# Kernel optimization log

Measured on AMD Instinct MI355X. Metric: run time of the kernel, lower is better.

Reference implementation:

```python
import itertools
import jax, jax.numpy as jnp
import numpy as np

N, C, D, S = 512, 128, 16, 10  # atoms, channels, irreps dim (0e+1o+2e+3o), species
IR_DIMS = {'0e': 1, '1o': 3}
MULS = {'0e': (23, 4, 1), '1o': (33, 6, 1)}  # path multiplicities for orders (3, 2, 1)


def _make_u(key, order, mul, ir_dim):
    # Synthetic stand-in for e3nn.reduced_symmetric_tensor_product_basis:
    # under permutation of the `order` leading D axes.
    shape = (D,) * order + (mul, ir_dim)
    u = jax.random.normal(key, shape, dtype=jnp.float32)
    mask = jax.random.bernoulli(jax.random.fold_in(key, 1), 0.1, shape)
    u = jnp.where(mask, u, 0.0)
    perms = list(itertools.permutations(range(order)))
    u = sum(jnp.transpose(u, p + (order, order + 1)) for p in perms) / len(perms)
    return u


def setup_inputs() -> dict:
    key = jax.random.key(0)
    ks = jax.random.split(key, 16)
    inp = {
        'x': jax.random.normal(ks[0], (N, C, D), dtype=jnp.float32),
        'index': jax.random.randint(ks[1], (N,), 0, S, dtype=jnp.int32),
    }
    i = 2
    for ir in IR_DIMS:
        for order, mul in zip((3, 2, 1), MULS[ir]):
            inp[f'u{order}_{ir}'] = _make_u(ks[i], order, mul, IR_DIMS[ir]); i += 1
            # gradient_normalization='element' -> init stddev mul**-0.5, no runtime scale
            inp[f'w{order}_{ir}'] = (jax.random.normal(ks[i], (S, mul, C), dtype=jnp.float32)
                                     * mul ** -0.5); i += 1
    return inp


def _contract(x, idx, u3, u2, u1, w3, w2, w1):
    # x: (N,C,D); uK: (D,)*K + (mulK, ir); wK: (S, mulK, C)
    w3i, w2i, w1i = w3[idx], w2[idx], w1[idx]  # species gather -> (N, mulK, C)
    # order 3: einsum('...jki,kc,cj->c...i', u3, w3i, x) batched over atoms.
    # Form p[n,c,k,j] = w3i[n,k,c]*x[n,c,j] first (small), then one big contraction.
    p = jnp.einsum('nkc,ncj->nckj', w3i, x)              # (N,C,mul3,D)
    out = jnp.einsum('abjki,nckj->ncabi', u3, p)         # (N,C,D,D,ir)
    # order 2: accumulate U2.w2, then contract one D axis with x
    out = out + jnp.einsum('abki,nkc->ncabi', u2, w2i)   # (N,C,D,D,ir)
    out = jnp.einsum('ncaji,ncj->ncai', out, x)          # (N,C,D,ir)
    # order 1: accumulate U1.w1, then final contraction with x
    out = out + jnp.einsum('aki,nkc->ncai', u1, w1i)     # (N,C,D,ir)
    out = jnp.einsum('ncji,ncj->nci', out, x)            # (N,C,ir)
    return out


def reference(x, index, u3_0e, w3_0e, u2_0e, w2_0e, u1_0e, w1_0e,
              u3_1o, w3_1o, u2_1o, w2_1o, u1_1o, w1_1o):
    out0 = _contract(x, index, u3_0e, u2_0e, u1_0e, w3_0e, w2_0e, w1_0e)  # (N,C,1)
    out1 = _contract(x, index, u3_1o, u2_1o, u1_1o, w3_1o, w2_1o, w1_1o)  # (N,C,3)
    return jnp.concatenate([out0, out1], axis=-1)  # (N,C,4) irreps 0e+1o
```

## Files before the change

kernel.cpp:

```cpp
#include <hip/hip_runtime.h>


#define DD     16
#define NATOM  512
#define NCH    128
#define NSPEC  10
#define NT3    816
#define NT2    136
#define NT     968
#define NTP    1024
#define ATB    16
#define APT    4
#define MAXB   42
#define CHUNKS 8
#define NTC    128
#define TILE   16
#define NTILES (NTC / TILE)
#define TPW    (TILE / 4)
#define CHALF  2
#define CT     8

#define WS_DESC  0
#define WS_ORDER 1024
#define WS_COEF  8192
#define COEF_BYTES (NSPEC * NTP * NCH * 16)
#define WS_PART  (WS_COEF + COEF_BYTES)

struct TermTable { unsigned v[NTP]; };
constexpr TermTable build_terms() {
  TermTable T{};
  int t = 0;
  for (int a = 0; a < DD; a++)
    for (int b = a; b < DD; b++)
      for (int j = b; j < DD; j++) {
        unsigned m = (a == b && b == j) ? 1u : ((a == b || b == j) ? 3u : 6u);
        T.v[t++] = (unsigned)(a | (b << 5) | (j << 10) | (3u << 15) | (m << 18));
      }
  for (int a = 0; a < DD; a++)
    for (int b = a; b < DD; b++) {
      unsigned m = (a == b) ? 1u : 2u;
      T.v[t++] = (unsigned)(a | (b << 5) | (16 << 10) | (2u << 15) | (m << 18));
    }
  for (int a = 0; a < DD; a++)
    T.v[t++] = (unsigned)(a | (16 << 5) | (16 << 10) | (1u << 15) | (1u << 18));
  while (t < NTP) T.v[t++] = (unsigned)(17 | (17 << 5) | (17 << 10));
  return T;
}
constexpr TermTable TERMS = build_terms();

__device__ void do_setup(const int* __restrict__ index, int* __restrict__ desc,
                         int* __restrict__ order) {
  __shared__ int cnt[NSPEC], cursor[NSPEC], bbase[NSPEC + 1];
  const int tid = threadIdx.x;
  if (tid < NSPEC) { cnt[tid] = 0; cursor[tid] = 0; }
  __syncthreads();
  for (int i = tid; i < NATOM; i += 128) atomicAdd(&cnt[index[i]], 1);
  for (int i = tid; i < MAXB * ATB; i += 128) order[i] = -1;
  __syncthreads();
  if (tid == 0) {
    int base = 0;
    for (int s = 0; s < NSPEC; s++) { bbase[s] = base; base += (cnt[s] + ATB - 1) / ATB; }
    bbase[NSPEC] = base;
  }
  __syncthreads();
  for (int i = tid; i < NATOM; i += 128) {
    int s = index[i];
    int pos = atomicAdd(&cursor[s], 1);
    order[bbase[s] * ATB + pos] = i;
  }
  for (int i = tid; i < MAXB; i += 128) {
    int sp = -1;
    for (int s = 0; s < NSPEC; s++)
      if (i >= bbase[s] && i < bbase[s + 1]) sp = s;
    desc[i] = sp;
  }
}

__global__ __launch_bounds__(128) void coef_setup_kernel(
    const float* __restrict__ u3_0, const float* __restrict__ w3_0,
    const float* __restrict__ u2_0, const float* __restrict__ w2_0,
    const float* __restrict__ u1_0, const float* __restrict__ w1_0,
    const float* __restrict__ u3_1, const float* __restrict__ w3_1,
    const float* __restrict__ u2_1, const float* __restrict__ w2_1,
    const float* __restrict__ u1_1, const float* __restrict__ w1_1,
    const int* __restrict__ index, int* __restrict__ desc,
    int* __restrict__ order, float* __restrict__ coef) {
  if (blockIdx.y == NTP / CT) {
    if (blockIdx.x == 0) do_setup(index, desc, order);
    return;
  }
  const int s = blockIdx.x;
  const int c = threadIdx.x;
  const int tbase = blockIdx.y * CT;

  __shared__ float us0[CT][23];
  __shared__ float us1[CT][99];

  for (int i = 0; i < CT; ++i) {
    const unsigned ev = TERMS.v[tbase + i];
    const int kind = (ev >> 15) & 7;
    const int a = ev & 31, b = (ev >> 5) & 31, j = (ev >> 10) & 31;
    if (kind == 3) {
      const int off = (a * DD + b) * DD + j;
      if (c < 23) us0[i][c] = u3_0[off * 23 + c];
      else if (c < 122) us1[i][c - 23] = u3_1[(size_t)off * 99 + (c - 23)];
    } else if (kind == 2) {
      const int off = a * DD + b;
      if (c < 4) us0[i][c] = u2_0[off * 4 + c];
      else if (c < 22) us1[i][c - 4] = u2_1[off * 18 + (c - 4)];
    } else if (kind == 1) {
      if (c < 1) us0[i][0] = u1_0[a];
      else if (c < 4) us1[i][c - 1] = u1_1[a * 3 + (c - 1)];
    }
  }
  __syncthreads();

  float r3_0[23], r3_1[33], r2_0[4], r2_1[6];
#pragma unroll
  for (int k = 0; k < 23; k++) r3_0[k] = w3_0[(s * 23 + k) * NCH + c];
#pragma unroll
  for (int k = 0; k < 33; k++) r3_1[k] = w3_1[(s * 33 + k) * NCH + c];
#pragma unroll
  for (int k = 0; k < 4; k++) r2_0[k] = w2_0[(s * 4 + k) * NCH + c];
#pragma unroll
  for (int k = 0; k < 6; k++) r2_1[k] = w2_1[(s * 6 + k) * NCH + c];
  const float r1_0 = w1_0[s * NCH + c];
  const float r1_1 = w1_1[s * NCH + c];

  for (int i = 0; i < CT; ++i) {
    const unsigned ev = TERMS.v[tbase + i];
    const int kind = (ev >> 15) & 7;
    const float fm = (float)((ev >> 18) & 7);
    float s0 = 0.f, s1 = 0.f, s2 = 0.f, s3 = 0.f;
    if (kind == 3) {
#pragma unroll
      for (int k = 0; k < 23; k++) s0 += us0[i][k] * r3_0[k];
#pragma unroll
      for (int k = 0; k < 33; k++) {
        const float w = r3_1[k];
        s1 += us1[i][k * 3 + 0] * w;
        s2 += us1[i][k * 3 + 1] * w;
        s3 += us1[i][k * 3 + 2] * w;
      }
    } else if (kind == 2) {
#pragma unroll
      for (int k = 0; k < 4; k++) s0 += us0[i][k] * r2_0[k];
#pragma unroll
      for (int k = 0; k < 6; k++) {
        const float w = r2_1[k];
        s1 += us1[i][k * 3 + 0] * w;
        s2 += us1[i][k * 3 + 1] * w;
        s3 += us1[i][k * 3 + 2] * w;
      }
    } else if (kind == 1) {
      s0 = us0[i][0] * r1_0;
      s1 = us1[i][0] * r1_1;
      s2 = us1[i][1] * r1_1;
      s3 = us1[i][2] * r1_1;
    }
    *(float4*)(coef + ((size_t)(s * NTP + tbase + i) * NCH + c) * 4) =
        float4{fm * s0, fm * s1, fm * s2, fm * s3};
  }
}

__device__ __forceinline__ void stage_tile(const float* __restrict__ lane_base,
                                           int t0_tile, float* dst_base, int wave) {
#pragma unroll
  for (int r = 0; r < TPW; ++r) {
    const int term = wave * TPW + r;
    const float* g = lane_base + (size_t)(t0_tile + term) * (NCH * 4);
    float* l = dst_base + term * 256;
    __builtin_amdgcn_global_load_lds(
        (const __attribute__((address_space(1))) unsigned int*)g,
        (__attribute__((address_space(3))) unsigned int*)l, 16, 0, 0);
  }
}

template <int CH>
__device__ __forceinline__ void eval_chunk(const float* __restrict__ lane_base,
                                           float (*lbuf)[TILE * 256],
                                           int wave, int lane,
                                           const float (&xr)[APT][18],
                                           float (&ac)[APT][4]) {
  constexpr int T0 = CH * NTC;
  stage_tile(lane_base, T0, &lbuf[0][0], wave);
#pragma unroll
  for (int tile = 0; tile < NTILES; ++tile) {
    __syncthreads();
    if (tile + 1 < NTILES)
      stage_tile(lane_base, T0 + (tile + 1) * TILE, &lbuf[(tile + 1) & 1][0], wave);
    const float* lb = &lbuf[tile & 1][0];
#pragma unroll
    for (int i = 0; i < TILE; ++i) {
      const unsigned ev = TERMS.v[T0 + tile * TILE + i];
      const int ea = ev & 31, eb = (ev >> 5) & 31, ej = (ev >> 10) & 31;
      const float4 cf = *(const float4*)(lb + (i * 64 + lane) * 4);
#pragma unroll
      for (int k = 0; k < APT; ++k) {
        const float m = xr[k][ea] * xr[k][eb] * xr[k][ej];
        ac[k][0] += cf.x * m; ac[k][1] += cf.y * m;
        ac[k][2] += cf.z * m; ac[k][3] += cf.w * m;
      }
    }
  }
}

__device__ __forceinline__ void load16(float (&xr)[18], const float* __restrict__ p) {
  const float4* q = (const float4*)p;
  const float4 v0 = q[0], v1 = q[1], v2 = q[2], v3 = q[3];
  xr[0] = v0.x; xr[1] = v0.y; xr[2] = v0.z; xr[3] = v0.w;
  xr[4] = v1.x; xr[5] = v1.y; xr[6] = v1.z; xr[7] = v1.w;
  xr[8] = v2.x; xr[9] = v2.y; xr[10] = v2.z; xr[11] = v2.w;
  xr[12] = v3.x; xr[13] = v3.y; xr[14] = v3.z; xr[15] = v3.w;
}

__global__ __launch_bounds__(256, 4) void contract_kernel(const float* __restrict__ x,
                                                          const int* __restrict__ desc,
                                                          const int* __restrict__ order,
                                                          const float* __restrict__ coef,
                                                          float* __restrict__ partial) {
  const int s = desc[blockIdx.x];
  if (s < 0) return;
  const int lane = threadIdx.x & 63;
  const int wave = threadIdx.x >> 6;
  const int c = blockIdx.z * 64 + lane;

  __shared__ float lbuf[2][TILE * 256];

  int n[APT];
#pragma unroll
  for (int k = 0; k < APT; k++) n[k] = order[blockIdx.x * ATB + wave * APT + k];

  float xr[APT][18];
#pragma unroll
  for (int k = 0; k < APT; k++) {
#pragma unroll
    for (int i = 0; i < DD; i++) xr[k][i] = 0.f;
    xr[k][16] = 1.f;
    xr[k][17] = 0.f;
  }
#pragma unroll
  for (int k = 0; k < APT; k++)
    if (n[k] >= 0) load16(xr[k], x + ((size_t)n[k] * NCH + c) * DD);

  float ac[APT][4];
#pragma unroll
  for (int k = 0; k < APT; k++) { ac[k][0] = 0.f; ac[k][1] = 0.f; ac[k][2] = 0.f; ac[k][3] = 0.f; }

  const float* lane_base = coef + ((size_t)s * NTP * NCH + (size_t)blockIdx.z * 64 + lane) * 4;

  switch (blockIdx.y) {
    case 0: eval_chunk<0>(lane_base, lbuf, wave, lane, xr, ac); break;
    case 1: eval_chunk<1>(lane_base, lbuf, wave, lane, xr, ac); break;
    case 2: eval_chunk<2>(lane_base, lbuf, wave, lane, xr, ac); break;
    case 3: eval_chunk<3>(lane_base, lbuf, wave, lane, xr, ac); break;
    case 4: eval_chunk<4>(lane_base, lbuf, wave, lane, xr, ac); break;
    case 5: eval_chunk<5>(lane_base, lbuf, wave, lane, xr, ac); break;
    case 6: eval_chunk<6>(lane_base, lbuf, wave, lane, xr, ac); break;
    default: eval_chunk<7>(lane_base, lbuf, wave, lane, xr, ac); break;
  }

  float* pb = partial + (size_t)blockIdx.y * (NATOM * NCH * 4);
#pragma unroll
  for (int k = 0; k < APT; k++)
    if (n[k] >= 0)
      *(float4*)(pb + ((size_t)n[k] * NCH + c) * 4) =
          float4{ac[k][0], ac[k][1], ac[k][2], ac[k][3]};
}

__global__ __launch_bounds__(256) void reduce_kernel(const float4* __restrict__ partial,
                                                     float4* __restrict__ out) {
  const int i = blockIdx.x * 256 + threadIdx.x;
  float4 s{0.f, 0.f, 0.f, 0.f};
#pragma unroll
  for (int ch = 0; ch < CHUNKS; ch++) {
    const float4 v = partial[(size_t)ch * (NATOM * NCH) + i];
    s.x += v.x; s.y += v.y; s.z += v.z; s.w += v.w;
  }
  out[i] = s;
}

extern "C" void kernel_launch(void* const* d_in, const int* in_sizes, int n_in,
                              void* d_out, int out_size, void* d_ws, size_t ws_size,
                              hipStream_t stream) {
  const float* x    = (const float*)d_in[0];
  const int* index  = (const int*)d_in[1];
  const float* u3_0 = (const float*)d_in[2];
  const float* w3_0 = (const float*)d_in[3];
  const float* u2_0 = (const float*)d_in[4];
  const float* w2_0 = (const float*)d_in[5];
  const float* u1_0 = (const float*)d_in[6];
  const float* w1_0 = (const float*)d_in[7];
  const float* u3_1 = (const float*)d_in[8];
  const float* w3_1 = (const float*)d_in[9];
  const float* u2_1 = (const float*)d_in[10];
  const float* w2_1 = (const float*)d_in[11];
  const float* u1_1 = (const float*)d_in[12];
  const float* w1_1 = (const float*)d_in[13];
  float* out = (float*)d_out;

  char* ws = (char*)d_ws;
  int* desc      = (int*)(ws + WS_DESC);
  int* order     = (int*)(ws + WS_ORDER);
  float* coef    = (float*)(ws + WS_COEF);
  float* partial = (float*)(ws + WS_PART);

  coef_setup_kernel<<<dim3(NSPEC, NTP / CT + 1), 128, 0, stream>>>(
      u3_0, w3_0, u2_0, w2_0, u1_0, w1_0,
      u3_1, w3_1, u2_1, w2_1, u1_1, w1_1, index, desc, order, coef);
  contract_kernel<<<dim3(MAXB, CHUNKS, CHALF), 256, 0, stream>>>(x, desc, order, coef, partial);
  reduce_kernel<<<(NATOM * NCH) / 256, 256, 0, stream>>>((const float4*)partial, (float4*)out);
}
```

Before: 159.5 us.

## Flatten grids with chunk-interleaved block order and halve LDS tile size

Both the coefficient-setup and contract kernels now use 1D grids, with the block index decoded so that consecutive blocks step through the 8 term chunks first. On MI355X this is meant to spread work for the same species and atoms across XCDs and CUs more evenly. The LDS staging tile is also halved from 16 to 8 terms, which cuts shared memory per block and can raise occupancy, at the cost of more tile iterations and barriers. The setup block moves to the last linear index of the grid.

```diff
diff --git a/kernel.cpp b/kernel.cpp
--- a/kernel.cpp
+++ b/kernel.cpp
@@ -14,11 +14,12 @@
 #define MAXB   42
 #define CHUNKS 8
 #define NTC    128
-#define TILE   16
+#define TILE   8
 #define NTILES (NTC / TILE)
 #define TPW    (TILE / 4)
 #define CHALF  2
 #define CT     8
+#define NBLK   (MAXB * CHUNKS * CHALF)
 
 #define WS_DESC  0
 #define WS_ORDER 1024
@@ -85,13 +86,16 @@
     const float* __restrict__ u1_1, const float* __restrict__ w1_1,
     const int* __restrict__ index, int* __restrict__ desc,
     int* __restrict__ order, float* __restrict__ coef) {
-  if (blockIdx.y == NTP / CT) {
-    if (blockIdx.x == 0) do_setup(index, desc, order);
+  if (blockIdx.x >= NSPEC * (NTP / CT)) {
+    do_setup(index, desc, order);
     return;
   }
-  const int s = blockIdx.x;
+  const int q   = blockIdx.x & 7;
+  const int idx = blockIdx.x >> 3;
+  const int s   = idx >> 4;
+  const int tyc = idx & 15;
+  const int tbase = (q * 16 + tyc) * CT;
   const int c = threadIdx.x;
-  const int tbase = blockIdx.y * CT;
 
   __shared__ float us0[CT][23];
   __shared__ float us1[CT][99];
@@ -219,17 +223,22 @@
                                                           const int* __restrict__ order,
                                                           const float* __restrict__ coef,
                                                           float* __restrict__ partial) {
-  const int s = desc[blockIdx.x];
+  const int lin   = blockIdx.x;
+  const int chunk = lin & 7;
+  const int idx   = lin >> 3;
+  const int half  = idx / MAXB;
+  const int bx    = idx % MAXB;
+  const int s = desc[bx];
   if (s < 0) return;
   const int lane = threadIdx.x & 63;
   const int wave = threadIdx.x >> 6;
-  const int c = blockIdx.z * 64 + lane;
+  const int c = half * 64 + lane;
 
   __shared__ float lbuf[2][TILE * 256];
 
   int n[APT];
 #pragma unroll
-  for (int k = 0; k < APT; k++) n[k] = order[blockIdx.x * ATB + wave * APT + k];
+  for (int k = 0; k < APT; k++) n[k] = order[bx * ATB + wave * APT + k];
 
   float xr[APT][18];
 #pragma unroll
@@ -247,9 +256,9 @@
 #pragma unroll
   for (int k = 0; k < APT; k++) { ac[k][0] = 0.f; ac[k][1] = 0.f; ac[k][2] = 0.f; ac[k][3] = 0.f; }
 
-  const float* lane_base = coef + ((size_t)s * NTP * NCH + (size_t)blockIdx.z * 64 + lane) * 4;
-
-  switch (blockIdx.y) {
+  const float* lane_base = coef + ((size_t)s * NTP * NCH + (size_t)half * 64 + lane) * 4;
+
+  switch (chunk) {
     case 0: eval_chunk<0>(lane_base, lbuf, wave, lane, xr, ac); break;
     case 1: eval_chunk<1>(lane_base, lbuf, wave, lane, xr, ac); break;
     case 2: eval_chunk<2>(lane_base, lbuf, wave, lane, xr, ac); break;
@@ -260,7 +269,7 @@
     default: eval_chunk<7>(lane_base, lbuf, wave, lane, xr, ac); break;
   }
 
-  float* pb = partial + (size_t)blockIdx.y * (NATOM * NCH * 4);
+  float* pb = partial + (size_t)chunk * (NATOM * NCH * 4);
 #pragma unroll
   for (int k = 0; k < APT; k++)
     if (n[k] >= 0)
@@ -305,9 +314,9 @@
   float* coef    = (float*)(ws + WS_COEF);
   float* partial = (float*)(ws + WS_PART);
 
-  coef_setup_kernel<<<dim3(NSPEC, NTP / CT + 1), 128, 0, stream>>>(
+  coef_setup_kernel<<<NSPEC * (NTP / CT) + 1, 128, 0, stream>>>(
       u3_0, w3_0, u2_0, w2_0, u1_0, w1_0,
       u3_1, w3_1, u2_1, w2_1, u1_1, w1_1, index, desc, order, coef);
-  contract_kernel<<<dim3(MAXB, CHUNKS, CHALF), 256, 0, stream>>>(x, desc, order, coef, partial);
+  contract_kernel<<<NBLK, 256, 0, stream>>>(x, desc, order, coef, partial);
   reduce_kernel<<<(NATOM * NCH) / 256, 256, 0, stream>>>((const float4*)partial, (float4*)out);
 }
```

Result: slower. 174.7 us (+9.5%).
